# Performance work log

Hardware: AMD Instinct MI355X
Metric: run time of the kernel (lower is better)

## Reference

```python
import jax, jax.numpy as jnp
import numpy as np

N_ATOMS = 100000
N_PAIRS = 3200000
N_PROP = 16
N_BASIS = 10
W = 16  # MLP width for pp/pi/ii nodes


def setup_inputs() -> dict:
    key = jax.random.key(0)
    ks = jax.random.split(key, 16)
    s = 0.1
    inp = {
        "ind_2": jax.random.randint(ks[0], (N_PAIRS, 2), 0, N_ATOMS),
        "p1": jax.random.normal(ks[1], (N_ATOMS, N_PROP), dtype=jnp.float32),
        "basis": jax.random.normal(ks[2], (N_PAIRS, N_BASIS), dtype=jnp.float32),
        # pp_pre: [16,16], bias=True
        "Wpre0": jax.random.normal(ks[3], (N_PROP, W), dtype=jnp.float32) * s,
        "bpre0": jnp.zeros((W,), dtype=jnp.float32),
        "Wpre1": jax.random.normal(ks[4], (W, W), dtype=jnp.float32) * s,
        "bpre1": jnp.zeros((W,), dtype=jnp.float32),
        # pi: input 2*W -> W -> W*n_basis, bias=True
        "Wpi0": jax.random.normal(ks[5], (2 * W, W), dtype=jnp.float32) * s,
        "bpi0": jnp.zeros((W,), dtype=jnp.float32),
        "Wpi1": jax.random.normal(ks[6], (W, W * N_BASIS), dtype=jnp.float32) * s,
        "bpi1": jnp.zeros((W * N_BASIS,), dtype=jnp.float32),
        # ii: [16,16], bias=False
        "Wii0": jax.random.normal(ks[7], (W, W), dtype=jnp.float32) * s,
        "Wii1": jax.random.normal(ks[8], (W, W), dtype=jnp.float32) * s,
        # pp_post: [16,16], bias=False
        "Wpost0": jax.random.normal(ks[9], (W, W), dtype=jnp.float32) * s,
        "Wpost1": jax.random.normal(ks[10], (W, W), dtype=jnp.float32) * s,
    }
    return inp


def reference(ind_2, p1, basis, Wpre0, bpre0, Wpre1, bpre1,
              Wpi0, bpi0, Wpi1, bpi1, Wii0, Wii1, Wpost0, Wpost1):
    act = jnp.tanh
    n_atoms = p1.shape[0]
    # pp_pre: per-atom FF (activation on every dense, bias=True)
    p1_in = act(p1 @ Wpre0 + bpre0)
    p1_in = act(p1_in @ Wpre1 + bpre1)
    # PI: gather pair endpoints, concat, MLP, contract with radial basis
    h = jnp.concatenate([p1_in[ind_2[:, 0]], p1_in[ind_2[:, 1]]], axis=-1)  # (P, 2W)
    h = act(h @ Wpi0 + bpi0)                                                # (P, W)
    h = act(h @ Wpi1 + bpi1)                                                # (P, W*n_basis)
    h = h.reshape(h.shape[0], -1, basis.shape[-1])                          # (P, W, n_basis)
    i_pair = jnp.einsum('pcb,pb->pc', h, basis)                             # (P, W)
    # II: pair-mixing FF (bias=False)
    i_pair = act(i_pair @ Wii0)
    i_pair = act(i_pair @ Wii1)
    # IP: scatter-sum pair features back to atoms at ind_2[:,0]
    p_sum = jax.ops.segment_sum(i_pair, ind_2[:, 0], num_segments=n_atoms)  # (A, W)
    # pp_post (bias=False)
    p1_new = act(p_sum @ Wpost0)
    p1_new = act(p1_new @ Wpost1)
    return (p1_new, i_pair)
```

## Files before the change

kernel.cpp:

```cpp
#include <hip/hip_runtime.h>

#define N_ATOMS 100000
#define N_PAIRS 3200000
#define N_PROP 16
#define N_BASIS 10
#define W 16
#define NT (N_PAIRS / 16)
#define SCAN_BLK 1024
#define NB ((N_ATOMS + SCAN_BLK - 1) / SCAN_BLK)

typedef short  s16x8 __attribute__((ext_vector_type(8)));
typedef float  f32x4 __attribute__((ext_vector_type(4)));

__device__ __forceinline__ float fast_tanh(float x) {
    float e = __builtin_amdgcn_exp2f(x * 2.88539008177792681f);
    return 1.0f - 2.0f * __builtin_amdgcn_rcpf(e + 1.0f);
}
__device__ __forceinline__ unsigned short bf16r(float f) {
    union { float f; unsigned u; } v; v.f = f;
    unsigned r = v.u + 0x7FFFu + ((v.u >> 16) & 1u);
    return (unsigned short)(r >> 16);
}
__device__ __forceinline__ float bf16f(unsigned short h) {
    union { unsigned u; float f; } v; v.u = ((unsigned)h) << 16; return v.f;
}

__global__ __launch_bounds__(256) void k_pp_pre(
    const float* __restrict__ p1,
    const float* __restrict__ W0, const float* __restrict__ b0,
    const float* __restrict__ W1, const float* __restrict__ b1,
    unsigned short* __restrict__ p1h, unsigned short* __restrict__ p1l)
{
    int a = blockIdx.x * 256 + threadIdx.x;
    if (a >= N_ATOMS) return;
    const float4* src = reinterpret_cast<const float4*>(p1 + (size_t)a * N_PROP);
    float4 v0 = src[0], v1 = src[1], v2 = src[2], v3 = src[3];
    float x[N_PROP] = {v0.x,v0.y,v0.z,v0.w, v1.x,v1.y,v1.z,v1.w,
                       v2.x,v2.y,v2.z,v2.w, v3.x,v3.y,v3.z,v3.w};
    float h[W];
#pragma unroll
    for (int c = 0; c < W; ++c) h[c] = b0[c];
#pragma unroll
    for (int k = 0; k < N_PROP; ++k)
#pragma unroll
        for (int c = 0; c < W; ++c) h[c] += x[k] * W0[k*W + c];
#pragma unroll
    for (int c = 0; c < W; ++c) h[c] = fast_tanh(h[c]);
    float y[W];
#pragma unroll
    for (int c = 0; c < W; ++c) y[c] = b1[c];
#pragma unroll
    for (int k = 0; k < W; ++k)
#pragma unroll
        for (int c = 0; c < W; ++c) y[c] += h[k] * W1[k*W + c];
    union { unsigned short u[8]; s16x8 v; } hi0, hi1, lo0, lo1;
#pragma unroll
    for (int c = 0; c < W; ++c) {
        float t = fast_tanh(y[c]);
        unsigned short hb = bf16r(t);
        unsigned short lb = bf16r(t - bf16f(hb));
        if (c < 8) { hi0.u[c] = hb; lo0.u[c] = lb; }
        else       { hi1.u[c-8] = hb; lo1.u[c-8] = lb; }
    }
    s16x8* dh = reinterpret_cast<s16x8*>(p1h + (size_t)a * W);
    s16x8* dl = reinterpret_cast<s16x8*>(p1l + (size_t)a * W);
    dh[0] = hi0.v; dh[1] = hi1.v;
    dl[0] = lo0.v; dl[1] = lo1.v;
}

__device__ __forceinline__ void exch_to_B(float x0, float x1, float x2, float x3,
                                          int r, int g, bool augment,
                                          s16x8& Bh, s16x8& Bl)
{
    unsigned short h0 = bf16r(x0), h1 = bf16r(x1), h2 = bf16r(x2), h3 = bf16r(x3);
    unsigned hw0 = (unsigned)h0 | ((unsigned)h1 << 16);
    unsigned hw1 = (unsigned)h2 | ((unsigned)h3 << 16);
    unsigned short l0 = bf16r(x0 - bf16f(h0)), l1 = bf16r(x1 - bf16f(h1));
    unsigned short l2 = bf16r(x2 - bf16f(h2)), l3 = bf16r(x3 - bf16f(h3));
    unsigned lw0 = (unsigned)l0 | ((unsigned)l1 << 16);
    unsigned lw1 = (unsigned)l2 | ((unsigned)l3 << 16);
    int t0 = (r + 32*g) & 63, t1 = (r + 32*g + 16) & 63;
    unsigned bw0 = (unsigned)__shfl((int)hw0, t0);
    unsigned bw1 = (unsigned)__shfl((int)hw1, t0);
    unsigned bw2 = (unsigned)__shfl((int)hw0, t1);
    unsigned bw3 = (unsigned)__shfl((int)hw1, t1);
    unsigned cw0 = (unsigned)__shfl((int)lw0, t0);
    unsigned cw1 = (unsigned)__shfl((int)lw1, t0);
    unsigned cw2 = (unsigned)__shfl((int)lw0, t1);
    unsigned cw3 = (unsigned)__shfl((int)lw1, t1);
    if (g >= 2) {
        bw0 = (augment && g == 2) ? 0x3F80u : 0u;
        bw1 = bw2 = bw3 = 0u;
        cw0 = cw1 = cw2 = cw3 = 0u;
    }
    union { unsigned u[4]; s16x8 v; } ph, pl;
    ph.u[0] = bw0; ph.u[1] = bw1; ph.u[2] = bw2; ph.u[3] = bw3;
    pl.u[0] = cw0; pl.u[1] = cw1; pl.u[2] = cw2; pl.u[3] = cw3;
    Bh = ph.v; Bl = pl.v;
}

__device__ __forceinline__ s16x8 exch_hi(float x0, float x1, float x2, float x3,
                                         int r, int g)
{
    unsigned short h0 = bf16r(x0), h1 = bf16r(x1), h2 = bf16r(x2), h3 = bf16r(x3);
    unsigned hw0 = (unsigned)h0 | ((unsigned)h1 << 16);
    unsigned hw1 = (unsigned)h2 | ((unsigned)h3 << 16);
    int t0 = (r + 32*g) & 63, t1 = (r + 32*g + 16) & 63;
    unsigned bw0 = (unsigned)__shfl((int)hw0, t0);
    unsigned bw1 = (unsigned)__shfl((int)hw1, t0);
    unsigned bw2 = (unsigned)__shfl((int)hw0, t1);
    unsigned bw3 = (unsigned)__shfl((int)hw1, t1);
    if (g >= 2) { bw0 = bw1 = bw2 = bw3 = 0u; }
    union { unsigned u[4]; s16x8 v; } ph;
    ph.u[0] = bw0; ph.u[1] = bw1; ph.u[2] = bw2; ph.u[3] = bw3;
    return ph.v;
}

template<int USE_RANK>
__global__ __launch_bounds__(256) void k_pair_mfma(
    const int*   __restrict__ ind2,
    const float* __restrict__ basis,
    const unsigned short* __restrict__ p1h,
    const unsigned short* __restrict__ p1l,
    const float* __restrict__ Wpi0, const float* __restrict__ bpi0,
    const float* __restrict__ Wpi1, const float* __restrict__ bpi1,
    const float* __restrict__ Wii0, const float* __restrict__ Wii1,
    float* __restrict__ i_pair_out,
    const unsigned* __restrict__ starts,
    const unsigned* __restrict__ rank,
    unsigned* __restrict__ cursor,
    float* __restrict__ svals)
{
    __shared__ s16x8 a2_lds[12][4][16];

    const int lane = threadIdx.x & 63;
    const int w    = threadIdx.x >> 6;
    const int r    = lane & 15;
    const int g    = lane >> 4;

    for (int e = threadIdx.x; e < 768; e += 256) {
        int t  = e >> 6;
        int rr = (e >> 2) & 15;
        int gg = e & 3;
        int ch = 4*(t & 3) + (rr >> 2);
        int bp = 4*(t >> 2) + (rr & 3);
        s16x8 val;
#pragma unroll
        for (int j = 0; j < 8; ++j) {
            int k = 8*gg + j;
            float wv = 0.0f;
            if (bp < N_BASIS) {
                if (k < W)       wv = Wpi1[k*(W*N_BASIS) + ch*N_BASIS + bp];
                else if (k == W) wv = bpi1[ch*N_BASIS + bp];
            }
            val[j] = (short)bf16r(wv);
        }
        a2_lds[t][gg][rr] = val;
    }

    s16x8 a1, a3, a4;
#pragma unroll
    for (int j = 0; j < 8; ++j) {
        int k = 8*g + j;
        a1[j] = (short)bf16r(Wpi0[k*W + r]);
        a3[j] = (short)(k < W ? bf16r(Wii0[k*W + r]) : 0);
        a4[j] = (short)(k < W ? bf16r(Wii1[k*W + r]) : 0);
    }
    float b0v[4];
#pragma unroll
    for (int i = 0; i < 4; ++i) b0v[i] = bpi0[4*g + i];

    __syncthreads();

    for (int tile = blockIdx.x * 4 + w; tile < NT; tile += gridDim.x * 4) {
        const int p0 = tile * 16;
        const int p  = p0 + r;
        int2 ij = reinterpret_cast<const int2*>(ind2)[p];
        int atom = (g < 2) ? ij.x : ij.y;

        const s16x8 B1h = *reinterpret_cast<const s16x8*>(p1h + (size_t)atom * W + (g & 1) * 8);
        const s16x8 B1l = *reinterpret_cast<const s16x8*>(p1l + (size_t)atom * W + (g & 1) * 8);

        const float2* bb = reinterpret_cast<const float2*>(basis + (size_t)p * N_BASIS);
        float bas[12];
#pragma unroll
        for (int q = 0; q < 5; ++q) { float2 t2 = bb[q]; bas[2*q] = t2.x; bas[2*q+1] = t2.y; }
        bas[10] = 0.0f; bas[11] = 0.0f;

        f32x4 acc = {0.f, 0.f, 0.f, 0.f};
        acc = __builtin_amdgcn_mfma_f32_16x16x32_bf16(a1, B1h, acc, 0, 0, 0);
        acc = __builtin_amdgcn_mfma_f32_16x16x32_bf16(a1, B1l, acc, 0, 0, 0);
        float h0v[4];
#pragma unroll
        for (int i = 0; i < 4; ++i) h0v[i] = fast_tanh(acc[i] + b0v[i]);

        s16x8 B2h, B2l;
        exch_to_B(h0v[0], h0v[1], h0v[2], h0v[3], r, g, true, B2h, B2l);

        float vloc[4] = {0.f, 0.f, 0.f, 0.f};
#pragma unroll
        for (int t = 0; t < 12; ++t) {
            s16x8 af = a2_lds[t][g][r];
            f32x4 z = {0.f, 0.f, 0.f, 0.f};
            z = __builtin_amdgcn_mfma_f32_16x16x32_bf16(af, B2h, z, 0, 0, 0);
            z = __builtin_amdgcn_mfma_f32_16x16x32_bf16(af, B2l, z, 0, 0, 0);
#pragma unroll
            for (int i = 0; i < 4; ++i)
                vloc[t & 3] += fast_tanh(z[i]) * bas[4*(t >> 2) + i];
        }
        float fm[16];
#pragma unroll
        for (int m = 0; m < 4; ++m)
#pragma unroll
            for (int q = 0; q < 4; ++q)
                fm[4*m + q] = __shfl(vloc[m], r + 16*q);

        s16x8 B3h;
        if (g == 0) {
#pragma unroll
            for (int j = 0; j < 8; ++j) B3h[j] = (short)bf16r(fm[j]);
        } else if (g == 1) {
#pragma unroll
            for (int j = 0; j < 8; ++j) B3h[j] = (short)bf16r(fm[8 + j]);
        } else {
#pragma unroll
            for (int j = 0; j < 8; ++j) B3h[j] = 0;
        }

        f32x4 ua = {0.f, 0.f, 0.f, 0.f};
        ua = __builtin_amdgcn_mfma_f32_16x16x32_bf16(a3, B3h, ua, 0, 0, 0);
        s16x8 B4h = exch_hi(fast_tanh(ua[0]), fast_tanh(ua[1]),
                            fast_tanh(ua[2]), fast_tanh(ua[3]), r, g);

        f32x4 wa = {0.f, 0.f, 0.f, 0.f};
        wa = __builtin_amdgcn_mfma_f32_16x16x32_bf16(a4, B4h, wa, 0, 0, 0);
        float4 outv = make_float4(fast_tanh(wa[0]), fast_tanh(wa[1]),
                                  fast_tanh(wa[2]), fast_tanh(wa[3]));
        *reinterpret_cast<float4*>(i_pair_out + (size_t)p * W + 4*g) = outv;

        unsigned pos;
        if (USE_RANK) {
            pos = starts[ij.x] + rank[p];
        } else {
            unsigned pp = 0;
            if (g == 0) pp = atomicAdd(&cursor[ij.x], 1u);
            pos = (unsigned)__shfl((int)pp, r);
        }
        *reinterpret_cast<float4*>(svals + (size_t)pos * W + 4*g) = outv;
    }
}

__global__ __launch_bounds__(256) void k_count(const int* __restrict__ ind2,
                                               unsigned* __restrict__ counts,
                                               unsigned* __restrict__ rank)
{
    int p = blockIdx.x * 256 + threadIdx.x;
    if (p >= N_PAIRS) return;
    rank[p] = atomicAdd(&counts[ind2[2*p]], 1u);
}

__global__ __launch_bounds__(SCAN_BLK) void k_scanA(const unsigned* __restrict__ counts,
                                                    unsigned* __restrict__ starts,
                                                    unsigned* __restrict__ bsum)
{
    __shared__ unsigned sc[SCAN_BLK];
    int a = blockIdx.x * SCAN_BLK + threadIdx.x;
    unsigned c = (a < N_ATOMS) ? counts[a] : 0u;
    sc[threadIdx.x] = c;
    __syncthreads();
    for (int off = 1; off < SCAN_BLK; off <<= 1) {
        unsigned v = sc[threadIdx.x];
        unsigned add = (threadIdx.x >= off) ? sc[threadIdx.x - off] : 0u;
        __syncthreads();
        sc[threadIdx.x] = v + add;
        __syncthreads();
    }
    if (a < N_ATOMS) starts[a] = sc[threadIdx.x] - c;
    if (threadIdx.x == SCAN_BLK - 1) bsum[blockIdx.x] = sc[SCAN_BLK - 1];
}

__global__ void k_scanB(unsigned* __restrict__ bsum, unsigned* __restrict__ boff)
{
    if (threadIdx.x == 0) {
        unsigned run = 0;
        for (int b = 0; b < NB; ++b) { boff[b] = run; run += bsum[b]; }
    }
}

__global__ __launch_bounds__(SCAN_BLK) void k_scanC(unsigned* __restrict__ starts,
                                                    const unsigned* __restrict__ boff,
                                                    unsigned* __restrict__ cursor)
{
    int a = blockIdx.x * SCAN_BLK + threadIdx.x;
    if (a >= N_ATOMS) return;
    unsigned s = starts[a] + boff[blockIdx.x];
    starts[a] = s;
    cursor[a] = s;
}

__global__ __launch_bounds__(256) void k_reduce_stream(const unsigned* __restrict__ starts,
                                                       const unsigned* __restrict__ counts,
                                                       const float* __restrict__ svals,
                                                       float* __restrict__ p_sum)
{
    int a = blockIdx.x * 4 + (threadIdx.x >> 6);
    if (a >= N_ATOMS) return;
    int lane = threadIdx.x & 63;
    int c = lane & 15, q = lane >> 4;
    unsigned n = counts[a], st = starts[a];
    float acc = 0.0f;
    for (unsigned k = q; k < n; k += 4)
        acc += svals[(size_t)(st + k) * W + c];
    acc += __shfl_xor(acc, 16);
    acc += __shfl_xor(acc, 32);
    if (q == 0) p_sum[(size_t)a * W + c] = acc;
}

__global__ __launch_bounds__(256) void k_pp_post(
    const float* __restrict__ p_sum,
    const float* __restrict__ W0, const float* __restrict__ W1,
    float* __restrict__ p1_new)
{
    int a = blockIdx.x * 256 + threadIdx.x;
    if (a >= N_ATOMS) return;
    const float4* src = reinterpret_cast<const float4*>(p_sum + (size_t)a * W);
    float4 v0 = src[0], v1 = src[1], v2 = src[2], v3 = src[3];
    float x[W] = {v0.x,v0.y,v0.z,v0.w, v1.x,v1.y,v1.z,v1.w,
                  v2.x,v2.y,v2.z,v2.w, v3.x,v3.y,v3.z,v3.w};
    float h[W];
#pragma unroll
    for (int c = 0; c < W; ++c) h[c] = 0.0f;
#pragma unroll
    for (int k = 0; k < W; ++k)
#pragma unroll
        for (int c = 0; c < W; ++c) h[c] += x[k] * W0[k*W + c];
#pragma unroll
    for (int c = 0; c < W; ++c) h[c] = fast_tanh(h[c]);
    float y[W];
#pragma unroll
    for (int c = 0; c < W; ++c) y[c] = 0.0f;
#pragma unroll
    for (int k = 0; k < W; ++k)
#pragma unroll
        for (int c = 0; c < W; ++c) y[c] += h[k] * W1[k*W + c];
    float4* dst = reinterpret_cast<float4*>(p1_new + (size_t)a * W);
    dst[0] = make_float4(fast_tanh(y[0]),  fast_tanh(y[1]),  fast_tanh(y[2]),  fast_tanh(y[3]));
    dst[1] = make_float4(fast_tanh(y[4]),  fast_tanh(y[5]),  fast_tanh(y[6]),  fast_tanh(y[7]));
    dst[2] = make_float4(fast_tanh(y[8]),  fast_tanh(y[9]),  fast_tanh(y[10]), fast_tanh(y[11]));
    dst[3] = make_float4(fast_tanh(y[12]), fast_tanh(y[13]), fast_tanh(y[14]), fast_tanh(y[15]));
}

extern "C" void kernel_launch(void* const* d_in, const int* in_sizes, int n_in,
                              void* d_out, int out_size, void* d_ws, size_t ws_size,
                              hipStream_t stream) {
    const int*   ind2   = (const int*)d_in[0];
    const float* p1     = (const float*)d_in[1];
    const float* basis  = (const float*)d_in[2];
    const float* Wpre0  = (const float*)d_in[3];
    const float* bpre0  = (const float*)d_in[4];
    const float* Wpre1  = (const float*)d_in[5];
    const float* bpre1  = (const float*)d_in[6];
    const float* Wpi0   = (const float*)d_in[7];
    const float* bpi0   = (const float*)d_in[8];
    const float* Wpi1   = (const float*)d_in[9];
    const float* bpi1   = (const float*)d_in[10];
    const float* Wii0   = (const float*)d_in[11];
    const float* Wii1   = (const float*)d_in[12];
    const float* Wpost0 = (const float*)d_in[13];
    const float* Wpost1 = (const float*)d_in[14];

    float* out    = (float*)d_out;
    float* p1_new = out;
    float* i_pair = out + (size_t)N_ATOMS * W;

    char* ws = (char*)d_ws;
    unsigned short* p1h = (unsigned short*)ws;                    ws += (size_t)N_ATOMS * W * 2;
    unsigned short* p1l = (unsigned short*)ws;                    ws += (size_t)N_ATOMS * W * 2;
    float*    p_sum  = (float*)ws;                                ws += (size_t)N_ATOMS * W * 4;
    unsigned* counts = (unsigned*)ws;                             ws += (size_t)N_ATOMS * 4;
    unsigned* starts = (unsigned*)ws;                             ws += (size_t)N_ATOMS * 4;
    unsigned* cursor = (unsigned*)ws;                             ws += (size_t)N_ATOMS * 4;
    unsigned* bsum   = (unsigned*)ws;                             ws += 1024 * 4;
    unsigned* boff   = (unsigned*)ws;                             ws += 1024 * 4;
    float*    svals  = (float*)ws;                                ws += (size_t)N_PAIRS * W * 4;
    unsigned* rank   = (unsigned*)ws;                             ws += (size_t)N_PAIRS * 4;

    int use_rank = (ws_size >= (size_t)(ws - (char*)d_ws));

    hipMemsetAsync(counts, 0, (size_t)N_ATOMS * sizeof(unsigned), stream);
    k_pp_pre<<<(N_ATOMS + 255) / 256, 256, 0, stream>>>(p1, Wpre0, bpre0, Wpre1, bpre1, p1h, p1l);
    k_count<<<(N_PAIRS + 255) / 256, 256, 0, stream>>>(ind2, counts, use_rank ? rank : cursor);
    k_scanA<<<NB, SCAN_BLK, 0, stream>>>(counts, starts, bsum);
    k_scanB<<<1, 64, 0, stream>>>(bsum, boff);
    k_scanC<<<NB, SCAN_BLK, 0, stream>>>(starts, boff, cursor);

    if (use_rank) {
        k_pair_mfma<1><<<2560, 256, 0, stream>>>(ind2, basis, p1h, p1l,
                                                 Wpi0, bpi0, Wpi1, bpi1, Wii0, Wii1,
                                                 i_pair, starts, rank, cursor, svals);
    } else {
        k_pair_mfma<0><<<2560, 256, 0, stream>>>(ind2, basis, p1h, p1l,
                                                 Wpi0, bpi0, Wpi1, bpi1, Wii0, Wii1,
                                                 i_pair, starts, rank, cursor, svals);
    }
    k_reduce_stream<<<(N_ATOMS + 3) / 4, 256, 0, stream>>>(starts, counts, svals, p_sum);
    k_pp_post<<<(N_ATOMS + 255) / 256, 256, 0, stream>>>(p_sum, Wpost0, Wpost1, p1_new);
}
```

Measured before the change: 581.1 us.

## Process two pair tiles per wave, fold tanh scale into weights, use packed bf16 convert

The pair kernel now handles two 16-pair tiles per iteration and interleaves their MFMA chains, giving more independent work to hide MFMA and load latency. The tanh prescale is folded into the bf16 weights and biases, removing a multiply per activation. Bf16 hi/lo splitting uses the hardware packed convert instruction instead of manual rounding, and the A2 channel layout is permuted so the basis-contracted results can be exchanged with the same shuffle helper. The single-thread block-offset scan is replaced with a parallel LDS scan. The main risk is higher register pressure from doubling the live state, which could lower occupancy.

```diff
diff --git a/kernel.cpp b/kernel.cpp
--- a/kernel.cpp
+++ b/kernel.cpp
@@ -6,14 +6,20 @@
 #define N_BASIS 10
 #define W 16
 #define NT (N_PAIRS / 16)
+#define NSUP (NT / 2)
 #define SCAN_BLK 1024
 #define NB ((N_ATOMS + SCAN_BLK - 1) / SCAN_BLK)
+#define SC 2.88539008177792681f
 
 typedef short  s16x8 __attribute__((ext_vector_type(8)));
 typedef float  f32x4 __attribute__((ext_vector_type(4)));
 
+__device__ __forceinline__ float tanh_pre(float y) {
+    float e = __builtin_amdgcn_exp2f(y);
+    return 1.0f - 2.0f * __builtin_amdgcn_rcpf(e + 1.0f);
+}
 __device__ __forceinline__ float fast_tanh(float x) {
-    float e = __builtin_amdgcn_exp2f(x * 2.88539008177792681f);
+    float e = __builtin_amdgcn_exp2f(x * SC);
     return 1.0f - 2.0f * __builtin_amdgcn_rcpf(e + 1.0f);
 }
 __device__ __forceinline__ unsigned short bf16r(float f) {
@@ -23,6 +29,14 @@
 }
 __device__ __forceinline__ float bf16f(unsigned short h) {
     union { unsigned u; float f; } v; v.u = ((unsigned)h) << 16; return v.f;
+}
+__device__ __forceinline__ unsigned cvt_pk_bf16(float a, float b) {
+    unsigned r;
+    asm("v_cvt_pk_bf16_f32 %0, %1, %2" : "=v"(r) : "v"(a), "v"(b));
+    return r;
+}
+__device__ __forceinline__ float bitf(unsigned u) {
+    union { unsigned u; float f; } v; v.u = u; return v.f;
 }
 
 __global__ __launch_bounds__(256) void k_pp_pre(
@@ -68,52 +82,32 @@
     dl[0] = lo0.v; dl[1] = lo1.v;
 }
 
-__device__ __forceinline__ void exch_to_B(float x0, float x1, float x2, float x3,
-                                          int r, int g, bool augment,
-                                          s16x8& Bh, s16x8& Bl)
-{
-    unsigned short h0 = bf16r(x0), h1 = bf16r(x1), h2 = bf16r(x2), h3 = bf16r(x3);
-    unsigned hw0 = (unsigned)h0 | ((unsigned)h1 << 16);
-    unsigned hw1 = (unsigned)h2 | ((unsigned)h3 << 16);
-    unsigned short l0 = bf16r(x0 - bf16f(h0)), l1 = bf16r(x1 - bf16f(h1));
-    unsigned short l2 = bf16r(x2 - bf16f(h2)), l3 = bf16r(x3 - bf16f(h3));
-    unsigned lw0 = (unsigned)l0 | ((unsigned)l1 << 16);
-    unsigned lw1 = (unsigned)l2 | ((unsigned)l3 << 16);
-    int t0 = (r + 32*g) & 63, t1 = (r + 32*g + 16) & 63;
-    unsigned bw0 = (unsigned)__shfl((int)hw0, t0);
-    unsigned bw1 = (unsigned)__shfl((int)hw1, t0);
-    unsigned bw2 = (unsigned)__shfl((int)hw0, t1);
-    unsigned bw3 = (unsigned)__shfl((int)hw1, t1);
-    unsigned cw0 = (unsigned)__shfl((int)lw0, t0);
-    unsigned cw1 = (unsigned)__shfl((int)lw1, t0);
-    unsigned cw2 = (unsigned)__shfl((int)lw0, t1);
-    unsigned cw3 = (unsigned)__shfl((int)lw1, t1);
-    if (g >= 2) {
-        bw0 = (augment && g == 2) ? 0x3F80u : 0u;
-        bw1 = bw2 = bw3 = 0u;
-        cw0 = cw1 = cw2 = cw3 = 0u;
-    }
-    union { unsigned u[4]; s16x8 v; } ph, pl;
-    ph.u[0] = bw0; ph.u[1] = bw1; ph.u[2] = bw2; ph.u[3] = bw3;
-    pl.u[0] = cw0; pl.u[1] = cw1; pl.u[2] = cw2; pl.u[3] = cw3;
-    Bh = ph.v; Bl = pl.v;
-}
-
-__device__ __forceinline__ s16x8 exch_hi(float x0, float x1, float x2, float x3,
-                                         int r, int g)
-{
-    unsigned short h0 = bf16r(x0), h1 = bf16r(x1), h2 = bf16r(x2), h3 = bf16r(x3);
-    unsigned hw0 = (unsigned)h0 | ((unsigned)h1 << 16);
-    unsigned hw1 = (unsigned)h2 | ((unsigned)h3 << 16);
-    int t0 = (r + 32*g) & 63, t1 = (r + 32*g + 16) & 63;
-    unsigned bw0 = (unsigned)__shfl((int)hw0, t0);
-    unsigned bw1 = (unsigned)__shfl((int)hw1, t0);
-    unsigned bw2 = (unsigned)__shfl((int)hw0, t1);
-    unsigned bw3 = (unsigned)__shfl((int)hw1, t1);
-    if (g >= 2) { bw0 = bw1 = bw2 = bw3 = 0u; }
-    union { unsigned u[4]; s16x8 v; } ph;
-    ph.u[0] = bw0; ph.u[1] = bw1; ph.u[2] = bw2; ph.u[3] = bw3;
-    return ph.v;
+__device__ __forceinline__ void make_B_hilo(const float x[4], int idxA, int idxB,
+                                            int g, bool augment, s16x8& Bh, s16x8& Bl)
+{
+    unsigned w0h = cvt_pk_bf16(x[0], x[1]);
+    unsigned w1h = cvt_pk_bf16(x[2], x[3]);
+    float f0 = bitf(w0h << 16), f1 = bitf(w0h & 0xFFFF0000u);
+    float f2 = bitf(w1h << 16), f3 = bitf(w1h & 0xFFFF0000u);
+    unsigned w0l = cvt_pk_bf16(x[0] - f0, x[1] - f1);
+    unsigned w1l = cvt_pk_bf16(x[2] - f2, x[3] - f3);
+    union { unsigned u[4]; s16x8 v; } H, L;
+    H.u[0] = (unsigned)__shfl((int)w0h, idxA); H.u[1] = (unsigned)__shfl((int)w1h, idxA);
+    H.u[2] = (unsigned)__shfl((int)w0h, idxB); H.u[3] = (unsigned)__shfl((int)w1h, idxB);
+    L.u[0] = (unsigned)__shfl((int)w0l, idxA); L.u[1] = (unsigned)__shfl((int)w1l, idxA);
+    L.u[2] = (unsigned)__shfl((int)w0l, idxB); L.u[3] = (unsigned)__shfl((int)w1l, idxB);
+    if (augment && g == 2) { H.u[0] = 0x3F80u; L.u[0] = 0u; }
+    Bh = H.v; Bl = L.v;
+}
+
+__device__ __forceinline__ s16x8 make_B_hi(const float x[4], int idxA, int idxB)
+{
+    unsigned w0 = cvt_pk_bf16(x[0], x[1]);
+    unsigned w1 = cvt_pk_bf16(x[2], x[3]);
+    union { unsigned u[4]; s16x8 v; } H;
+    H.u[0] = (unsigned)__shfl((int)w0, idxA); H.u[1] = (unsigned)__shfl((int)w1, idxA);
+    H.u[2] = (unsigned)__shfl((int)w0, idxB); H.u[3] = (unsigned)__shfl((int)w1, idxB);
+    return H.v;
 }
 
 template<int USE_RANK>
@@ -137,12 +131,14 @@
     const int w    = threadIdx.x >> 6;
     const int r    = lane & 15;
     const int g    = lane >> 4;
+    const int idxA = (r + 32*g) & 63;
+    const int idxB = (idxA + 16) & 63;
 
     for (int e = threadIdx.x; e < 768; e += 256) {
         int t  = e >> 6;
         int rr = (e >> 2) & 15;
         int gg = e & 3;
-        int ch = 4*(t & 3) + (rr >> 2);
+        int ch = 4*(rr >> 2) + (t & 3);
         int bp = 4*(t >> 2) + (rr & 3);
         s16x8 val;
 #pragma unroll
@@ -153,7 +149,7 @@
                 if (k < W)       wv = Wpi1[k*(W*N_BASIS) + ch*N_BASIS + bp];
                 else if (k == W) wv = bpi1[ch*N_BASIS + bp];
             }
-            val[j] = (short)bf16r(wv);
+            val[j] = (short)bf16r(SC * wv);
         }
         a2_lds[t][gg][rr] = val;
     }
@@ -162,91 +158,116 @@
 #pragma unroll
     for (int j = 0; j < 8; ++j) {
         int k = 8*g + j;
-        a1[j] = (short)bf16r(Wpi0[k*W + r]);
-        a3[j] = (short)(k < W ? bf16r(Wii0[k*W + r]) : 0);
-        a4[j] = (short)(k < W ? bf16r(Wii1[k*W + r]) : 0);
+        a1[j] = (short)bf16r(SC * Wpi0[k*W + r]);
+        a3[j] = (short)(k < W ? bf16r(SC * Wii0[k*W + r]) : 0);
+        a4[j] = (short)(k < W ? bf16r(SC * Wii1[k*W + r]) : 0);
     }
     float b0v[4];
 #pragma unroll
-    for (int i = 0; i < 4; ++i) b0v[i] = bpi0[4*g + i];
+    for (int i = 0; i < 4; ++i) b0v[i] = SC * bpi0[4*g + i];
 
     __syncthreads();
 
-    for (int tile = blockIdx.x * 4 + w; tile < NT; tile += gridDim.x * 4) {
-        const int p0 = tile * 16;
-        const int p  = p0 + r;
-        int2 ij = reinterpret_cast<const int2*>(ind2)[p];
-        int atom = (g < 2) ? ij.x : ij.y;
-
-        const s16x8 B1h = *reinterpret_cast<const s16x8*>(p1h + (size_t)atom * W + (g & 1) * 8);
-        const s16x8 B1l = *reinterpret_cast<const s16x8*>(p1l + (size_t)atom * W + (g & 1) * 8);
-
-        const float2* bb = reinterpret_cast<const float2*>(basis + (size_t)p * N_BASIS);
-        float bas[12];
-#pragma unroll
-        for (int q = 0; q < 5; ++q) { float2 t2 = bb[q]; bas[2*q] = t2.x; bas[2*q+1] = t2.y; }
-        bas[10] = 0.0f; bas[11] = 0.0f;
-
-        f32x4 acc = {0.f, 0.f, 0.f, 0.f};
-        acc = __builtin_amdgcn_mfma_f32_16x16x32_bf16(a1, B1h, acc, 0, 0, 0);
-        acc = __builtin_amdgcn_mfma_f32_16x16x32_bf16(a1, B1l, acc, 0, 0, 0);
-        float h0v[4];
-#pragma unroll
-        for (int i = 0; i < 4; ++i) h0v[i] = fast_tanh(acc[i] + b0v[i]);
-
-        s16x8 B2h, B2l;
-        exch_to_B(h0v[0], h0v[1], h0v[2], h0v[3], r, g, true, B2h, B2l);
-
-        float vloc[4] = {0.f, 0.f, 0.f, 0.f};
+    for (int sup = blockIdx.x * 4 + w; sup < NSUP; sup += gridDim.x * 4) {
+        const int pA = sup * 32 + r;
+        const int pB = pA + 16;
+        int2 ijA = reinterpret_cast<const int2*>(ind2)[pA];
+        int2 ijB = reinterpret_cast<const int2*>(ind2)[pB];
+        int atomA = (g < 2) ? ijA.x : ijA.y;
+        int atomB = (g < 2) ? ijB.x : ijB.y;
+
+        const s16x8 B1hA = *reinterpret_cast<const s16x8*>(p1h + (size_t)atomA * W + (g & 1) * 8);
+        const s16x8 B1lA = *reinterpret_cast<const s16x8*>(p1l + (size_t)atomA * W + (g & 1) * 8);
+        const s16x8 B1hB = *reinterpret_cast<const s16x8*>(p1h + (size_t)atomB * W + (g & 1) * 8);
+        const s16x8 B1lB = *reinterpret_cast<const s16x8*>(p1l + (size_t)atomB * W + (g & 1) * 8);
+
+        float basA[12], basB[12];
+        {
+            const float2* bbA = reinterpret_cast<const float2*>(basis + (size_t)pA * N_BASIS);
+            const float2* bbB = reinterpret_cast<const float2*>(basis + (size_t)pB * N_BASIS);
+#pragma unroll
+            for (int q = 0; q < 5; ++q) {
+                float2 tA = bbA[q]; basA[2*q] = tA.x; basA[2*q+1] = tA.y;
+                float2 tB = bbB[q]; basB[2*q] = tB.x; basB[2*q+1] = tB.y;
+            }
+            basA[10] = basA[11] = 0.0f;
+            basB[10] = basB[11] = 0.0f;
+        }
+
+        f32x4 accA = {0.f,0.f,0.f,0.f}, accB = {0.f,0.f,0.f,0.f};
+        accA = __builtin_amdgcn_mfma_f32_16x16x32_bf16(a1, B1hA, accA, 0, 0, 0);
+        accB = __builtin_amdgcn_mfma_f32_16x16x32_bf16(a1, B1hB, accB, 0, 0, 0);
+        accA = __builtin_amdgcn_mfma_f32_16x16x32_bf16(a1, B1lA, accA, 0, 0, 0);
+        accB = __builtin_amdgcn_mfma_f32_16x16x32_bf16(a1, B1lB, accB, 0, 0, 0);
+        float h0A[4], h0B[4];
+#pragma unroll
+        for (int i = 0; i < 4; ++i) {
+            h0A[i] = tanh_pre(accA[i] + b0v[i]);
+            h0B[i] = tanh_pre(accB[i] + b0v[i]);
+        }
+
+        s16x8 B2hA, B2lA, B2hB, B2lB;
+        make_B_hilo(h0A, idxA, idxB, g, true, B2hA, B2lA);
+        make_B_hilo(h0B, idxA, idxB, g, true, B2hB, B2lB);
+
+        float vlA[4] = {0.f,0.f,0.f,0.f}, vlB[4] = {0.f,0.f,0.f,0.f};
 #pragma unroll
         for (int t = 0; t < 12; ++t) {
             s16x8 af = a2_lds[t][g][r];
-            f32x4 z = {0.f, 0.f, 0.f, 0.f};
-            z = __builtin_amdgcn_mfma_f32_16x16x32_bf16(af, B2h, z, 0, 0, 0);
-            z = __builtin_amdgcn_mfma_f32_16x16x32_bf16(af, B2l, z, 0, 0, 0);
-#pragma unroll
-            for (int i = 0; i < 4; ++i)
-                vloc[t & 3] += fast_tanh(z[i]) * bas[4*(t >> 2) + i];
-        }
-        float fm[16];
-#pragma unroll
-        for (int m = 0; m < 4; ++m)
-#pragma unroll
-            for (int q = 0; q < 4; ++q)
-                fm[4*m + q] = __shfl(vloc[m], r + 16*q);
-
-        s16x8 B3h;
-        if (g == 0) {
-#pragma unroll
-            for (int j = 0; j < 8; ++j) B3h[j] = (short)bf16r(fm[j]);
-        } else if (g == 1) {
-#pragma unroll
-            for (int j = 0; j < 8; ++j) B3h[j] = (short)bf16r(fm[8 + j]);
+            f32x4 zA = {0.f,0.f,0.f,0.f}, zB = {0.f,0.f,0.f,0.f};
+            zA = __builtin_amdgcn_mfma_f32_16x16x32_bf16(af, B2hA, zA, 0, 0, 0);
+            zB = __builtin_amdgcn_mfma_f32_16x16x32_bf16(af, B2hB, zB, 0, 0, 0);
+            zA = __builtin_amdgcn_mfma_f32_16x16x32_bf16(af, B2lA, zA, 0, 0, 0);
+            zB = __builtin_amdgcn_mfma_f32_16x16x32_bf16(af, B2lB, zB, 0, 0, 0);
+#pragma unroll
+            for (int i = 0; i < 4; ++i) {
+                const int bi = 4*(t >> 2) + i;
+                const int m  = t & 3;
+                vlA[m] += tanh_pre(zA[i]) * basA[bi];
+                vlB[m] += tanh_pre(zB[i]) * basB[bi];
+            }
+        }
+
+        s16x8 B3hA = make_B_hi(vlA, idxA, idxB);
+        s16x8 B3hB = make_B_hi(vlB, idxA, idxB);
+        f32x4 uaA = {0.f,0.f,0.f,0.f}, uaB = {0.f,0.f,0.f,0.f};
+        uaA = __builtin_amdgcn_mfma_f32_16x16x32_bf16(a3, B3hA, uaA, 0, 0, 0);
+        uaB = __builtin_amdgcn_mfma_f32_16x16x32_bf16(a3, B3hB, uaB, 0, 0, 0);
+        float tuA[4], tuB[4];
+#pragma unroll
+        for (int i = 0; i < 4; ++i) {
+            tuA[i] = tanh_pre(uaA[i]);
+            tuB[i] = tanh_pre(uaB[i]);
+        }
+
+        s16x8 B4hA = make_B_hi(tuA, idxA, idxB);
+        s16x8 B4hB = make_B_hi(tuB, idxA, idxB);
+        f32x4 waA = {0.f,0.f,0.f,0.f}, waB = {0.f,0.f,0.f,0.f};
+        waA = __builtin_amdgcn_mfma_f32_16x16x32_bf16(a4, B4hA, waA, 0, 0, 0);
+        waB = __builtin_amdgcn_mfma_f32_16x16x32_bf16(a4, B4hB, waB, 0, 0, 0);
+        float4 outA = make_float4(tanh_pre(waA[0]), tanh_pre(waA[1]),
+                                  tanh_pre(waA[2]), tanh_pre(waA[3]));
+        float4 outB = make_float4(tanh_pre(waB[0]), tanh_pre(waB[1]),
+                                  tanh_pre(waB[2]), tanh_pre(waB[3]));
+
+        *reinterpret_cast<float4*>(i_pair_out + (size_t)pA * W + 4*g) = outA;
+        *reinterpret_cast<float4*>(i_pair_out + (size_t)pB * W + 4*g) = outB;
+
+        unsigned posA, posB;
+        if (USE_RANK) {
+            posA = starts[ijA.x] + rank[pA];
+            posB = starts[ijB.x] + rank[pB];
         } else {
-#pragma unroll
-            for (int j = 0; j < 8; ++j) B3h[j] = 0;
-        }
-
-        f32x4 ua = {0.f, 0.f, 0.f, 0.f};
-        ua = __builtin_amdgcn_mfma_f32_16x16x32_bf16(a3, B3h, ua, 0, 0, 0);
-        s16x8 B4h = exch_hi(fast_tanh(ua[0]), fast_tanh(ua[1]),
-                            fast_tanh(ua[2]), fast_tanh(ua[3]), r, g);
-
-        f32x4 wa = {0.f, 0.f, 0.f, 0.f};
-        wa = __builtin_amdgcn_mfma_f32_16x16x32_bf16(a4, B4h, wa, 0, 0, 0);
-        float4 outv = make_float4(fast_tanh(wa[0]), fast_tanh(wa[1]),
-                                  fast_tanh(wa[2]), fast_tanh(wa[3]));
-        *reinterpret_cast<float4*>(i_pair_out + (size_t)p * W + 4*g) = outv;
-
-        unsigned pos;
-        if (USE_RANK) {
-            pos = starts[ij.x] + rank[p];
-        } else {
-            unsigned pp = 0;
-            if (g == 0) pp = atomicAdd(&cursor[ij.x], 1u);
-            pos = (unsigned)__shfl((int)pp, r);
-        }
-        *reinterpret_cast<float4*>(svals + (size_t)pos * W + 4*g) = outv;
+            unsigned ppA = 0, ppB = 0;
+            if (g == 0) {
+                ppA = atomicAdd(&cursor[ijA.x], 1u);
+                ppB = atomicAdd(&cursor[ijB.x], 1u);
+            }
+            posA = (unsigned)__shfl((int)ppA, r);
+            posB = (unsigned)__shfl((int)ppB, r);
+        }
+        *reinterpret_cast<float4*>(svals + (size_t)posA * W + 4*g) = outA;
+        *reinterpret_cast<float4*>(svals + (size_t)posB * W + 4*g) = outB;
     }
 }
 
@@ -279,12 +300,22 @@
     if (threadIdx.x == SCAN_BLK - 1) bsum[blockIdx.x] = sc[SCAN_BLK - 1];
 }
 
-__global__ void k_scanB(unsigned* __restrict__ bsum, unsigned* __restrict__ boff)
-{
-    if (threadIdx.x == 0) {
-        unsigned run = 0;
-        for (int b = 0; b < NB; ++b) { boff[b] = run; run += bsum[b]; }
-    }
+__global__ __launch_bounds__(128) void k_scanB(const unsigned* __restrict__ bsum,
+                                               unsigned* __restrict__ boff)
+{
+    __shared__ unsigned s[128];
+    int t = threadIdx.x;
+    unsigned v = (t < NB) ? bsum[t] : 0u;
+    s[t] = v;
+    __syncthreads();
+    for (int off = 1; off < 128; off <<= 1) {
+        unsigned x = s[t];
+        unsigned add = (t >= off) ? s[t - off] : 0u;
+        __syncthreads();
+        s[t] = x + add;
+        __syncthreads();
+    }
+    if (t < NB) boff[t] = s[t] - v;
 }
 
 __global__ __launch_bounds__(SCAN_BLK) void k_scanC(unsigned* __restrict__ starts,
@@ -391,7 +422,7 @@
     k_pp_pre<<<(N_ATOMS + 255) / 256, 256, 0, stream>>>(p1, Wpre0, bpre0, Wpre1, bpre1, p1h, p1l);
     k_count<<<(N_PAIRS + 255) / 256, 256, 0, stream>>>(ind2, counts, use_rank ? rank : cursor);
     k_scanA<<<NB, SCAN_BLK, 0, stream>>>(counts, starts, bsum);
-    k_scanB<<<1, 64, 0, stream>>>(bsum, boff);
+    k_scanB<<<1, 128, 0, stream>>>(bsum, boff);
     k_scanC<<<NB, SCAN_BLK, 0, stream>>>(starts, boff, cursor);
 
     if (use_rank) {
```

After: 584.9 us. About the same (+0.7%).
